# Kernel optimization log

Measured on AMD Instinct MI355X. Metric: run time of the kernel, lower is better.

The kernel has to match this reference:

```python
import jax, jax.numpy as jnp
import numpy as np

B, S, D, H, E, K = 4, 1024, 1024, 16, 8, 2
DH = D // H
FF = 4 * D  # expert hidden dim
EPS = 1e-5


def _layernorm(x, g, b):
    mu = jnp.mean(x, axis=-1, keepdims=True)
    var = jnp.mean(jnp.square(x - mu), axis=-1, keepdims=True)
    return (x - mu) / jnp.sqrt(var + EPS) * g + b


def setup_inputs() -> dict:
    key = jax.random.key(0)
    ks = jax.random.split(key, 16)
    s = 0.02
    return {
        "x": jax.random.normal(ks[0], (B, S, D), jnp.float32),
        "mask": jnp.ones((B, S), jnp.int32),
        "ln1_g": jnp.ones((D,), jnp.float32),
        "ln1_b": jnp.zeros((D,), jnp.float32),
        "ln2_g": jnp.ones((D,), jnp.float32),
        "ln2_b": jnp.zeros((D,), jnp.float32),
        "wq": jax.random.normal(ks[1], (D, D), jnp.float32) * s,
        "bq": jnp.zeros((D,), jnp.float32),
        "wk": jax.random.normal(ks[2], (D, D), jnp.float32) * s,
        "bk": jnp.zeros((D,), jnp.float32),
        "wv": jax.random.normal(ks[3], (D, D), jnp.float32) * s,
        "bv": jnp.zeros((D,), jnp.float32),
        "wo": jax.random.normal(ks[4], (D, D), jnp.float32) * s,
        "bo": jnp.zeros((D,), jnp.float32),
        "w_router": jax.random.normal(ks[5], (D, E), jnp.float32) * s,
        "b_router": jnp.zeros((E,), jnp.float32),
        "w1": jax.random.normal(ks[6], (E, D, FF), jnp.float32) * s,
        "b1": jnp.zeros((E, FF), jnp.float32),
        "w2": jax.random.normal(ks[7], (E, FF, D), jnp.float32) * s,
        "b2": jnp.zeros((E, D), jnp.float32),
    }


def _forward(x, mask, ln1_g, ln1_b, ln2_g, ln2_b, wq, bq, wk, bk, wv, bv,
             wo, bo, w_router, b_router, w1, b1, w2, b2):
    scale = DH ** -0.5
    # --- attention sub-block (pre-LN) ---
    xn = _layernorm(x, ln1_g, ln1_b)
    q = (xn @ wq + bq).reshape(B, S, H, DH).transpose(0, 2, 1, 3)  # [B,H,S,DH]
    k = (xn @ wk + bk).reshape(B, S, H, DH).transpose(0, 2, 1, 3)
    v = (xn @ wv + bv).reshape(B, S, H, DH).transpose(0, 2, 1, 3)
    scores = jnp.einsum('bhqd,bhkd->bhqk', q, k) * scale
    scores = jnp.where(mask[:, None, None, :] == 0, -jnp.inf, scores)
    attn = jax.nn.softmax(scores, axis=-1)
    ao = jnp.einsum('bhqk,bhkd->bhqd', attn, v)
    ao = ao.transpose(0, 2, 1, 3).reshape(B, S, D) @ wo + bo
    x = x + ao  # dropout is identity in eval
    # --- MoE sub-block ---
    xn2 = _layernorm(x, ln2_g, ln2_b)
    logits = xn2 @ w_router + b_router          # [B,S,E]
    top_v, top_i = jax.lax.top_k(logits, K)     # [B,S,K]
    probs = jax.nn.softmax(top_v, axis=-1)      # softmax over top-k logits
    # dense combine weight per expert: sum_k prob_k * onehot(idx_k)
    combine = jnp.sum(jax.nn.one_hot(top_i, E, dtype=xn2.dtype) * probs[..., None], axis=-2)  # [B,S,E]
    h = jax.nn.gelu(jnp.einsum('bsd,edh->ebsh', xn2, w1) + b1[:, None, None, :], approximate=False)
    eo = jnp.einsum('ebsh,ehd->ebsd', h, w2) + b2[:, None, None, :]   # [E,B,S,D]
    moe_out = jnp.einsum('bse,ebsd->bsd', combine, eo)
    return x + moe_out


def reference(x, mask, ln1_g, ln1_b, ln2_g, ln2_b, wq, bq, wk, bk, wv, bv,
              wo, bo, w_router, b_router, w1, b1, w2, b2):
    return _forward(x, mask, ln1_g, ln1_b, ln2_g, ln2_b, wq, bq, wk, bk, wv,
                    bv, wo, bo, w_router, b_router, w1, b1, w2, b2)
```

## Files before the change

kernel.cpp:

```cpp
#include <hip/hip_runtime.h>
#include <hip/hip_bf16.h>
#include <cmath>

typedef __hip_bfloat16 bf16;
typedef float f32x4 __attribute__((ext_vector_type(4)));
typedef int   i32x4 __attribute__((ext_vector_type(4)));

#define DEV static __device__ __forceinline__

constexpr int BB   = 4;
constexpr int SS   = 1024;
constexpr int DM   = 1024;
constexpr int HH   = 16;
constexpr int DHD  = 64;
constexpr int NEXP = 8;
constexpr int FFD  = 4096;
constexpr int NTOK = BB*SS;
constexpr int CAP  = NTOK*2 + NEXP*128;

DEV float bf2f(unsigned short u){ union{unsigned int i; float f;} z; z.i=((unsigned int)u)<<16; return z.f; }
DEV unsigned short f2bf(float f){ bf16 h = __float2bfloat16(f); return __builtin_bit_cast(unsigned short, h); }

DEV void stage16(const void* g, void* lds_base_uniform) {
  __builtin_amdgcn_global_load_lds(
      (const __attribute__((address_space(1))) void*)g,
      (__attribute__((address_space(3))) void*)lds_base_uniform,
      16, 0, 0);
}

template<int BM,int BN,int EPI,bool EXPERT,bool GATHER,bool OUT_SLOT,int NPASS=1,int ZMODE=0>
__global__ __launch_bounds__((BM/64)*(BN/64)*64)
void et_gemm(const bf16* __restrict__ A, const bf16* __restrict__ Bt, void* __restrict__ Cout,
             const float* __restrict__ bias, const float* __restrict__ res,
             int Kdim, int lda, int ldb, int ldc,
             long abs_, long bbs_, long cbs_, float scale,
             const int* __restrict__ pad_off, const int* __restrict__ slots,
             long psA, long psB, float* __restrict__ Cf, int bias_zs)
{
  constexpr int WN = BN/64, WM = BM/64, NW = WM*WN;
  constexpr int CA = (BM/16)/NW, CB = (BN/16)/NW;
  const int tid = threadIdx.x, wid = tid>>6, lane = tid&63;

  const int gx = gridDim.x, gy = gridDim.y;
  const long nwg = (long)gx*gy*gridDim.z;
  long lin = blockIdx.x + (long)gx*(blockIdx.y + (long)gy*blockIdx.z);
  {
    const long q = nwg >> 3, r = nwg & 7;
    const long xcd = lin & 7, idx = lin >> 3;
    lin = (xcd < r ? xcd*(q+1) : r*(q+1) + (xcd-r)*q) + idx;
  }
  const int bxi = (int)(lin % gx);
  const long rem = lin / gx;
  const int byi = (int)(rem % gy);
  const int bzi = (int)(rem / gy);

  const int row0 = bxi*BM, col0 = byi*BN;
  const int z = bzi;
  int off0 = 0;
  if constexpr (EXPERT) {
    off0 = pad_off[z];
    const int rows = pad_off[z+1] - off0;
    if (row0 >= rows) return;
  }
  long coff;
  if constexpr (ZMODE==2) {
    A  += (long)z*SS*SS;
    Bt += (long)z*DHD*SS;
    coff = (long)(z>>4)*SS*DM + (long)(z&15)*64;
  } else {
    if constexpr (!EXPERT) A += (size_t)z * abs_;
    Bt += (size_t)z * bbs_;
    coff = (long)z*cbs_;
  }
  const long bofs = (long)z * bias_zs;

  const int sr = lane>>2;
  const int sk = (lane&3)*8;

  long arow[CA];
  #pragma unroll
  for (int i=0;i<CA;i++){
    const int r = (wid + i*NW)*16 + sr;
    if constexpr (GATHER)      arow[i] = slots[off0 + row0 + r];
    else if constexpr (EXPERT) arow[i] = off0 + row0 + r;
    else                       arow[i] = row0 + r;
  }
  int brow[CB];
  #pragma unroll
  for (int i=0;i<CB;i++) brow[i] = col0 + (wid + i*NW)*16 + sr;

  const int wm = wid / WN, wn = wid % WN;
  const int fr = lane & 15, fg = lane >> 4;

  f32x4 acc[4][4];
  #pragma unroll
  for (int m=0;m<4;m++)
    #pragma unroll
    for (int n=0;n<4;n++) acc[m][n] = (f32x4)(0.f);

  if constexpr (NPASS==3) {
    __shared__ __align__(16) bf16 As[2][2][BM*32];
    __shared__ __align__(16) bf16 Bs[2][2][BN*32];
    auto STG = [&](int buf, int kt) {
      #pragma unroll
      for (int i=0;i<CA;i++){
        stage16(A +        arow[i]*(long)lda + kt + sk, (void*)&As[buf][0][(wid + i*NW)*512]);
        stage16(A + psA +  arow[i]*(long)lda + kt + sk, (void*)&As[buf][1][(wid + i*NW)*512]);
      }
      #pragma unroll
      for (int i=0;i<CB;i++){
        stage16(Bt +       (long)brow[i]*ldb + kt + sk, (void*)&Bs[buf][0][(wid + i*NW)*512]);
        stage16(Bt + psB + (long)brow[i]*ldb + kt + sk, (void*)&Bs[buf][1][(wid + i*NW)*512]);
      }
    };
    const int nsteps = Kdim >> 5;
    int cur = 0;
    STG(0, 0);
    __syncthreads();
    for (int s = 0; s < nsteps; s++) {
      if (s + 1 < nsteps) STG(cur^1, (s+1)*32);
      i32x4 a0[4], a1[4], b0[4], b1[4];
      #pragma unroll
      for (int m=0;m<4;m++) {
        a0[m] = *(const i32x4*)&As[cur][0][(wm*64 + m*16 + fr)*32 + fg*8];
        a1[m] = *(const i32x4*)&As[cur][1][(wm*64 + m*16 + fr)*32 + fg*8];
      }
      #pragma unroll
      for (int n=0;n<4;n++) {
        b0[n] = *(const i32x4*)&Bs[cur][0][(wn*64 + n*16 + fr)*32 + fg*8];
        b1[n] = *(const i32x4*)&Bs[cur][1][(wn*64 + n*16 + fr)*32 + fg*8];
      }
      asm volatile("s_nop 1" ::);
      #pragma unroll
      for (int m=0;m<4;m++)
        #pragma unroll
        for (int n=0;n<4;n++) {
          asm("v_mfma_f32_16x16x32_bf16 %0, %1, %2, %0"
              : "+v"(acc[m][n]) : "v"(a0[m]), "v"(b0[n]));
          asm("v_mfma_f32_16x16x32_bf16 %0, %1, %2, %0"
              : "+v"(acc[m][n]) : "v"(a0[m]), "v"(b1[n]));
          asm("v_mfma_f32_16x16x32_bf16 %0, %1, %2, %0"
              : "+v"(acc[m][n]) : "v"(a1[m]), "v"(b0[n]));
        }
      __syncthreads();
      cur ^= 1;
    }
  } else {
    __shared__ __align__(16) bf16 As[2][BM*32];
    __shared__ __align__(16) bf16 Bs[2][BN*32];
    auto STAGE = [&](int buf, int kt) {
      #pragma unroll
      for (int i=0;i<CA;i++)
        stage16(A + arow[i]*(long)lda + kt + sk, (void*)&As[buf][(wid + i*NW)*512]);
      #pragma unroll
      for (int i=0;i<CB;i++)
        stage16(Bt + (long)brow[i]*ldb + kt + sk, (void*)&Bs[buf][(wid + i*NW)*512]);
    };
    const int nsteps = Kdim >> 5;
    int cur = 0;
    STAGE(0, 0);
    __syncthreads();
    for (int s = 0; s < nsteps; s++) {
      if (s + 1 < nsteps) STAGE(cur^1, (s+1)*32);
      i32x4 av[4], bv[4];
      #pragma unroll
      for (int m=0;m<4;m++) av[m] = *(const i32x4*)&As[cur][(wm*64 + m*16 + fr)*32 + fg*8];
      #pragma unroll
      for (int n=0;n<4;n++) bv[n] = *(const i32x4*)&Bs[cur][(wn*64 + n*16 + fr)*32 + fg*8];
      asm volatile("s_nop 1" ::);
      #pragma unroll
      for (int m=0;m<4;m++)
        #pragma unroll
        for (int n=0;n<4;n++)
          asm("v_mfma_f32_16x16x32_bf16 %0, %1, %2, %0"
              : "+v"(acc[m][n]) : "v"(av[m]), "v"(bv[n]));
      __syncthreads();
      cur ^= 1;
    }
  }

  #pragma unroll
  for (int m=0;m<4;m++)
    #pragma unroll
    for (int n=0;n<4;n++)
      asm volatile("s_nop 7\n\ts_nop 7" : "+v"(acc[m][n]) ::);

  const long rbase = (EXPERT && OUT_SLOT) ? (long)(off0 + row0) : (long)row0;
  #pragma unroll
  for (int m=0;m<4;m++) {
    #pragma unroll
    for (int n=0;n<4;n++) {
      #pragma unroll
      for (int j=0;j<4;j++) {
        const long r = rbase + wm*64 + m*16 + fg*4 + j;
        const long c = col0 + wn*64 + n*16 + fr;
        const size_t ci = (size_t)coff + (size_t)r*ldc + c;
        float v = acc[m][n][j];
        if constexpr (EPI==0) {
          ((bf16*)Cout)[ci] = __float2bfloat16(v + bias[bofs + c]);
        } else if constexpr (EPI==1) {
          ((bf16*)Cout)[ci] = __float2bfloat16(v*scale);
        } else if constexpr (EPI==2) {
          ((float*)Cout)[ci] = v + bias[bofs + c] + res[(size_t)r*ldc + c];
        } else if constexpr (EPI==3) {
          const float t = v + bias[bofs + c];
          ((bf16*)Cout)[ci] = __float2bfloat16(0.5f*t*(1.0f+erff(t*0.70710678118654752f)));
        } else {
          const float t = v + bias[bofs + c];
          ((bf16*)Cout)[ci] = __float2bfloat16(t);
          Cf[ci] = t;
        }
      }
    }
  }
}

__global__ __launch_bounds__(256)
void k_flash(const bf16* __restrict__ qb, const bf16* __restrict__ kb,
             const bf16* __restrict__ vt, const int* __restrict__ mask,
             bf16* __restrict__ aob)
{
  const int qt = blockIdx.x, h = blockIdx.y, b = blockIdx.z;
  const int tid = threadIdx.x, wid = tid>>6, lane = tid&63;
  const int fr = lane & 15, fg = lane >> 4;
  __shared__ __align__(16) bf16 Ks[64*64];
  __shared__ __align__(16) bf16 Vs[64*64];
  __shared__ __align__(16) bf16 Pl[4][16*64];
  const int q0 = qt*64;
  const int qrow = q0 + wid*16 + fr;
  i32x4 qreg[2];
  #pragma unroll
  for (int c=0;c<2;c++)
    qreg[c] = *(const i32x4*)&qb[((size_t)(b*SS)+qrow)*DM + h*64 + c*32 + fg*8];
  f32x4 oacc[4];
  #pragma unroll
  for (int n=0;n<4;n++) oacc[n]=(f32x4)(0.f);
  float mrow[4], lrow[4];
  #pragma unroll
  for (int j=0;j<4;j++){ mrow[j]=-1e30f; lrow[j]=0.f; }

  const int srow = lane>>3;
  const int scolsw = ((lane&7) ^ srow)*8;
  auto swz = [](int row, int coleb)->int {
    return row*128 + (coleb ^ ((row&7)<<4));
  };

  for (int kt=0; kt<SS/64; kt++) {
    const int kv0 = kt*64;
    #pragma unroll
    for (int i=0;i<2;i++) {
      const int r = (wid*2+i)*8 + srow;
      stage16(kb + ((size_t)(b*SS)+kv0+r)*DM + h*64 + scolsw, (void*)&Ks[(wid*2+i)*512]);
      stage16(vt + ((size_t)(b*HH+h)*64 + r)*SS + kv0 + scolsw, (void*)&Vs[(wid*2+i)*512]);
    }
    __syncthreads();
    f32x4 sacc[4];
    #pragma unroll
    for (int n=0;n<4;n++) sacc[n]=(f32x4)(0.f);
    asm volatile("s_nop 1" ::);
    #pragma unroll
    for (int c=0;c<2;c++) {
      i32x4 bk[4];
      #pragma unroll
      for (int n=0;n<4;n++)
        bk[n] = *(const i32x4*)((const char*)Ks + swz(n*16+fr, c*64+fg*16));
      #pragma unroll
      for (int n=0;n<4;n++)
        asm("v_mfma_f32_16x16x32_bf16 %0, %1, %2, %0"
            : "+v"(sacc[n]) : "v"(qreg[c]), "v"(bk[n]));
    }
    #pragma unroll
    for (int n=0;n<4;n++)
      asm volatile("s_nop 7\n\ts_nop 7" : "+v"(sacc[n]) ::);
    float sc[4][4];
    #pragma unroll
    for (int n=0;n<4;n++) {
      const bool mm = mask[b*SS + kv0 + n*16 + fr] != 0;
      #pragma unroll
      for (int j=0;j<4;j++)
        sc[n][j] = mm ? sacc[n][j]*0.125f : -1e30f;
    }
    float scale[4];
    #pragma unroll
    for (int j=0;j<4;j++) {
      float tm = fmaxf(fmaxf(sc[0][j],sc[1][j]),fmaxf(sc[2][j],sc[3][j]));
      #pragma unroll
      for (int o=8;o;o>>=1) tm = fmaxf(tm, __shfl_xor(tm,o));
      const float nm = fmaxf(mrow[j], tm);
      scale[j] = __expf(mrow[j]-nm);
      mrow[j] = nm;
      float ts = 0.f;
      #pragma unroll
      for (int n=0;n<4;n++) { sc[n][j] = __expf(sc[n][j]-nm); ts += sc[n][j]; }
      #pragma unroll
      for (int o=8;o;o>>=1) ts += __shfl_xor(ts,o);
      lrow[j] = lrow[j]*scale[j] + ts;
    }
    #pragma unroll
    for (int n=0;n<4;n++)
      asm volatile("s_nop 7\n\ts_nop 7" : "+v"(oacc[n]) ::);
    #pragma unroll
    for (int n=0;n<4;n++)
      #pragma unroll
      for (int j=0;j<4;j++) oacc[n][j] *= scale[j];
    char* plw = (char*)Pl[wid];
    #pragma unroll
    for (int n=0;n<4;n++)
      #pragma unroll
      for (int j=0;j<4;j++) {
        const int row = fg*4+j, col = n*16+fr;
        *(bf16*)(plw + row*128 + ((col*2) ^ ((row&7)<<4))) = __float2bfloat16(sc[n][j]);
      }
    asm volatile("s_nop 1" ::);
    #pragma unroll
    for (int c=0;c<2;c++) {
      i32x4 pa = *(const i32x4*)(plw + swz(fr, c*64+fg*16));
      i32x4 bv[4];
      #pragma unroll
      for (int n=0;n<4;n++)
        bv[n] = *(const i32x4*)((const char*)Vs + swz(n*16+fr, c*64+fg*16));
      #pragma unroll
      for (int n=0;n<4;n++)
        asm("v_mfma_f32_16x16x32_bf16 %0, %1, %2, %0"
            : "+v"(oacc[n]) : "v"(pa), "v"(bv[n]));
    }
    __syncthreads();
  }
  #pragma unroll
  for (int n=0;n<4;n++)
    asm volatile("s_nop 7\n\ts_nop 7" : "+v"(oacc[n]) ::);
  #pragma unroll
  for (int j=0;j<4;j++) {
    const float ri = 1.0f / lrow[j];
    const size_t rbase = ((size_t)(b*SS) + q0 + wid*16 + fg*4 + j)*DM + h*64;
    #pragma unroll
    for (int n=0;n<4;n++)
      aob[rbase + n*16 + fr] = __float2bfloat16(oacc[n][j] * ri);
  }
}

template<typename T>
__global__ __launch_bounds__(256)
void et_transpose(const T* __restrict__ in, bf16* __restrict__ outp,
                  int ldin, int ldout, long in_bs, long out_bs)
{
  __shared__ float tile[64][65];
  const int z = blockIdx.z;
  in   += (size_t)z * in_bs;
  outp += (size_t)z * out_bs;
  const int r0 = blockIdx.x*64, c0 = blockIdx.y*64;
  const int tid = threadIdx.x;
  #pragma unroll
  for (int i=0;i<4;i++) {
    const int idx = tid*4 + i*1024;
    const int r = idx>>6, c = idx&63;
    if constexpr (sizeof(T)==4) {
      const float4 v = *(const float4*)&in[(size_t)(r0+r)*ldin + c0 + c];
      tile[r][c]=v.x; tile[r][c+1]=v.y; tile[r][c+2]=v.z; tile[r][c+3]=v.w;
    } else {
      const ushort4 v = *(const ushort4*)&in[(size_t)(r0+r)*ldin + c0 + c];
      tile[r][c]=bf2f(v.x); tile[r][c+1]=bf2f(v.y); tile[r][c+2]=bf2f(v.z); tile[r][c+3]=bf2f(v.w);
    }
  }
  __syncthreads();
  #pragma unroll
  for (int i=0;i<4;i++) {
    const int idx = tid*4 + i*1024;
    const int c = idx>>6, r = idx&63;
    ushort4 o;
    o.x=f2bf(tile[r][c]); o.y=f2bf(tile[r+1][c]); o.z=f2bf(tile[r+2][c]); o.w=f2bf(tile[r+3][c]);
    *(ushort4*)&outp[(size_t)(c0+c)*ldout + r0 + r] = o;
  }
}

template<typename TI, typename TO>
__global__ __launch_bounds__(256)
void k_trans_head(const TI* __restrict__ in, TO* __restrict__ outp)
{
  __shared__ float tile[64][65];
  const int z = blockIdx.z;
  in   += (size_t)(z>>4)*SS*DM + (size_t)(z&15)*64;
  outp += (size_t)z*DHD*SS;
  const int r0 = blockIdx.x*64;
  const int tid = threadIdx.x;
  #pragma unroll
  for (int i=0;i<4;i++) {
    const int idx = tid*4 + i*1024;
    const int r = idx>>6, c = idx&63;
    if constexpr (sizeof(TI)==4) {
      const float4 v = *(const float4*)&in[(size_t)(r0+r)*DM + c];
      tile[r][c]=v.x; tile[r][c+1]=v.y; tile[r][c+2]=v.z; tile[r][c+3]=v.w;
    } else {
      const ushort4 v = *(const ushort4*)&in[(size_t)(r0+r)*DM + c];
      tile[r][c]=bf2f(v.x); tile[r][c+1]=bf2f(v.y); tile[r][c+2]=bf2f(v.z); tile[r][c+3]=bf2f(v.w);
    }
  }
  __syncthreads();
  #pragma unroll
  for (int i=0;i<4;i++) {
    const int idx = tid*4 + i*1024;
    const int c = idx>>6, r = idx&63;
    if constexpr (sizeof(TO)==4) {
      float4 o;
      o.x=tile[r][c]; o.y=tile[r+1][c]; o.z=tile[r+2][c]; o.w=tile[r+3][c];
      *(float4*)&outp[(size_t)c*SS + r0 + r] = o;
    } else {
      ushort4 o;
      o.x=f2bf(tile[r][c]); o.y=f2bf(tile[r+1][c]); o.z=f2bf(tile[r+2][c]); o.w=f2bf(tile[r+3][c]);
      *(ushort4*)&outp[(size_t)c*SS + r0 + r] = o;
    }
  }
}

__global__ __launch_bounds__(256)
void et_transpose2(const float* __restrict__ in0, const float* __restrict__ in1,
                   const float* __restrict__ in2, bf16* __restrict__ outp,
                   int ldin, int ldout, long pstride, long out_zs)
{
  __shared__ float tile[64][65];
  const int z = blockIdx.z;
  const float* in = (z==0) ? in0 : (z==1) ? in1 : in2;
  outp += (size_t)z * out_zs;
  const int r0 = blockIdx.x*64, c0 = blockIdx.y*64;
  const int tid = threadIdx.x;
  #pragma unroll
  for (int i=0;i<4;i++) {
    const int idx = tid*4 + i*1024;
    const int r = idx>>6, c = idx&63;
    const float4 v = *(const float4*)&in[(size_t)(r0+r)*ldin + c0 + c];
    tile[r][c]=v.x; tile[r][c+1]=v.y; tile[r][c+2]=v.z; tile[r][c+3]=v.w;
  }
  __syncthreads();
  #pragma unroll
  for (int i=0;i<4;i++) {
    const int idx = tid*4 + i*1024;
    const int c = idx>>6, r = idx&63;
    ushort4 o0, o1;
    unsigned short* p0 = (unsigned short*)&o0;
    unsigned short* p1 = (unsigned short*)&o1;
    #pragma unroll
    for (int j=0;j<4;j++) {
      float v = tile[r+j][c];
      const unsigned short h0 = f2bf(v);
      p0[j] = h0;
      v -= bf2f(h0);
      p1[j] = f2bf(v);
    }
    const size_t oi = (size_t)(c0+c)*ldout + r0 + r;
    *(ushort4*)&outp[oi] = o0;
    *(ushort4*)&outp[oi + pstride] = o1;
  }
}

__global__ __launch_bounds__(256)
void et_ln2(const float* __restrict__ xin, const float* __restrict__ g,
            const float* __restrict__ bsh, bf16* __restrict__ outp, long pstride)
{
  const int row = blockIdx.x, tid = threadIdx.x;
  const float4 v = ((const float4*)(xin + (size_t)row*DM))[tid];
  float s = v.x+v.y+v.z+v.w;
  #pragma unroll
  for (int o=32;o;o>>=1) s += __shfl_xor(s,o);
  __shared__ float s4[4], q4[4];
  if ((tid&63)==0) s4[tid>>6]=s;
  __syncthreads();
  const float mu = (s4[0]+s4[1]+s4[2]+s4[3]) * (1.f/DM);
  const float d0=v.x-mu,d1=v.y-mu,d2=v.z-mu,d3=v.w-mu;
  float q = d0*d0+d1*d1+d2*d2+d3*d3;
  #pragma unroll
  for (int o=32;o;o>>=1) q += __shfl_xor(q,o);
  if ((tid&63)==0) q4[tid>>6]=q;
  __syncthreads();
  const float var = (q4[0]+q4[1]+q4[2]+q4[3]) * (1.f/DM);
  const float rstd = rsqrtf(var + 1e-5f);
  const float4 gg = ((const float4*)g)[tid];
  const float4 bb = ((const float4*)bsh)[tid];
  float of[4];
  of[0] = d0*rstd*gg.x + bb.x;
  of[1] = d1*rstd*gg.y + bb.y;
  of[2] = d2*rstd*gg.z + bb.z;
  of[3] = d3*rstd*gg.w + bb.w;
  ushort4 p0, p1;
  unsigned short* pp0 = (unsigned short*)&p0;
  unsigned short* pp1 = (unsigned short*)&p1;
  #pragma unroll
  for (int k=0;k<4;k++) {
    float vv = of[k];
    const unsigned short h0 = f2bf(vv); pp0[k] = h0;
    vv -= bf2f(h0);
    pp1[k] = f2bf(vv);
  }
  const size_t oi = (size_t)row*DM;
  ((ushort4*)(outp + oi))[tid] = p0;
  ((ushort4*)(outp + pstride + oi))[tid] = p1;
}

__global__ __launch_bounds__(256)
void et_router2(const float* __restrict__ x1, const float* __restrict__ g,
                const float* __restrict__ bsh, const float* __restrict__ wr,
                const float* __restrict__ br, bf16* __restrict__ xn2,
                int* __restrict__ t2e, float* __restrict__ t2p,
                int* __restrict__ flaglist, int* __restrict__ cntb)
{
  const int wid = threadIdx.x>>6, lane = threadIdx.x&63;
  const int t = blockIdx.x*4 + wid;
  const float* xr = x1 + (size_t)t*DM;
  float4 xv[4];
  float s = 0.f;
  #pragma unroll
  for (int p=0;p<4;p++){
    xv[p] = *(const float4*)&xr[p*256 + lane*4];
    s += xv[p].x+xv[p].y+xv[p].z+xv[p].w;
  }
  #pragma unroll
  for (int o=32;o;o>>=1) s += __shfl_xor(s,o);
  const float mu = s * (1.f/DM);
  float q = 0.f;
  #pragma unroll
  for (int p=0;p<4;p++){
    const float a=xv[p].x-mu,b=xv[p].y-mu,c=xv[p].z-mu,d=xv[p].w-mu;
    q += a*a+b*b+c*c+d*d;
  }
  #pragma unroll
  for (int o=32;o;o>>=1) q += __shfl_xor(q,o);
  const float rstd = rsqrtf(q*(1.f/DM) + 1e-5f);
  float acc[NEXP];
  #pragma unroll
  for (int e=0;e<NEXP;e++) acc[e]=0.f;
  #pragma unroll
  for (int p=0;p<4;p++){
    const int d0 = p*256 + lane*4;
    const float4 gg = *(const float4*)&g[d0];
    const float4 bb = *(const float4*)&bsh[d0];
    float xn[4];
    xn[0]=(xv[p].x-mu)*rstd*gg.x+bb.x;
    xn[1]=(xv[p].y-mu)*rstd*gg.y+bb.y;
    xn[2]=(xv[p].z-mu)*rstd*gg.z+bb.z;
    xn[3]=(xv[p].w-mu)*rstd*gg.w+bb.w;
    ushort4 xo;
    xo.x=f2bf(xn[0]); xo.y=f2bf(xn[1]); xo.z=f2bf(xn[2]); xo.w=f2bf(xn[3]);
    *(ushort4*)&xn2[(size_t)t*DM + d0] = xo;
    #pragma unroll
    for (int j=0;j<4;j++){
      const float4 w0  = ((const float4*)&wr[(size_t)(d0+j)*NEXP])[0];
      const float4 w1v = ((const float4*)&wr[(size_t)(d0+j)*NEXP])[1];
      acc[0]+=xn[j]*w0.x;  acc[1]+=xn[j]*w0.y;  acc[2]+=xn[j]*w0.z;  acc[3]+=xn[j]*w0.w;
      acc[4]+=xn[j]*w1v.x; acc[5]+=xn[j]*w1v.y; acc[6]+=xn[j]*w1v.z; acc[7]+=xn[j]*w1v.w;
    }
  }
  #pragma unroll
  for (int e=0;e<NEXP;e++)
    #pragma unroll
    for (int o=32;o;o>>=1) acc[e] += __shfl_xor(acc[e],o);
  if (lane==0) {
    float v0=-1e30f, v1=-1e30f, v2=-1e30f; int e0=0, e1=0;
    #pragma unroll
    for (int e=0;e<NEXP;e++) {
      const float v = acc[e] + br[e];
      if (v>v0){v2=v1;v1=v0;e1=e0;v0=v;e0=e;}
      else if (v>v1){v2=v1;v1=v;e1=e;}
      else if (v>v2){v2=v;}
    }
    const float dd = __expf(v1-v0);
    const float p0 = 1.f/(1.f+dd);
    t2e[t*2]=e0; t2e[t*2+1]=e1;
    t2p[t*2]=p0; t2p[t*2+1]=dd*p0;
    if (v1 - v2 < 0.02f) {
      const int b = t >> 10;
      const int ib = atomicAdd(&cntb[b], 1);
      flaglist[b*1024 + ib] = t;
    }
  }
}

__global__ __launch_bounds__(256)
void k_rec4(const float* __restrict__ qf, const float* __restrict__ kfT,
            const float* __restrict__ vf, const int* __restrict__ flaglist,
            const int* __restrict__ cntb, const int* __restrict__ mask,
            float* __restrict__ aoF)
{
  const int h = blockIdx.y, b = blockIdx.z;
  const int tid = threadIdx.x, lane = tid&63, wv_ = tid>>6;
  const int nb = cntb[b];
  __shared__ float qs[4][64];
  __shared__ float scb[4][SS];
  __shared__ float part[4][4][64];
  __shared__ float tsum[4];
  const int* mrow = mask + (size_t)b*SS;
  const float* kbase = kfT + ((size_t)(b*HH + h)*DHD)*SS + tid;
  const float* vbase = vf + (size_t)b*SS*DM + h*64 + lane;

  for (int t0 = blockIdx.x*4; t0 < nb; t0 += gridDim.x*4) {
    const int nt = min(4, nb - t0);
    for (int idx = tid; idx < 4*64; idx += 256) {
      const int j = idx >> 6, d = idx & 63;
      float qv = 0.f;
      if (j < nt) {
        const int t = flaglist[b*1024 + t0 + j];
        qv = qf[(size_t)t*DM + h*64 + d];
      }
      qs[j][d] = qv;
    }
    __syncthreads();
    float a00=0,a01=0,a02=0,a03=0, a10=0,a11=0,a12=0,a13=0;
    float a20=0,a21=0,a22=0,a23=0, a30=0,a31=0,a32=0,a33=0;
    #pragma unroll 4
    for (int u=0; u<64; u++) {
      const float* kr = kbase + (size_t)u*SS;
      const float k0 = kr[0], k1 = kr[256], k2 = kr[512], k3 = kr[768];
      const float q0 = qs[0][u], q1 = qs[1][u], q2 = qs[2][u], q3 = qs[3][u];
      a00 += q0*k0; a01 += q0*k1; a02 += q0*k2; a03 += q0*k3;
      a10 += q1*k0; a11 += q1*k1; a12 += q1*k2; a13 += q1*k3;
      a20 += q2*k0; a21 += q2*k1; a22 += q2*k2; a23 += q2*k3;
      a30 += q3*k0; a31 += q3*k1; a32 += q3*k2; a33 += q3*k3;
    }
    const bool m0 = mrow[tid]!=0, m1 = mrow[tid+256]!=0, m2 = mrow[tid+512]!=0, m3 = mrow[tid+768]!=0;
    scb[0][tid]=m0?a00*0.125f:-1e30f; scb[0][tid+256]=m1?a01*0.125f:-1e30f;
    scb[0][tid+512]=m2?a02*0.125f:-1e30f; scb[0][tid+768]=m3?a03*0.125f:-1e30f;
    scb[1][tid]=m0?a10*0.125f:-1e30f; scb[1][tid+256]=m1?a11*0.125f:-1e30f;
    scb[1][tid+512]=m2?a12*0.125f:-1e30f; scb[1][tid+768]=m3?a13*0.125f:-1e30f;
    scb[2][tid]=m0?a20*0.125f:-1e30f; scb[2][tid+256]=m1?a21*0.125f:-1e30f;
    scb[2][tid+512]=m2?a22*0.125f:-1e30f; scb[2][tid+768]=m3?a23*0.125f:-1e30f;
    scb[3][tid]=m0?a30*0.125f:-1e30f; scb[3][tid+256]=m1?a31*0.125f:-1e30f;
    scb[3][tid+512]=m2?a32*0.125f:-1e30f; scb[3][tid+768]=m3?a33*0.125f:-1e30f;
    __syncthreads();
    {
      const int j = wv_;
      float v[16];
      float lm = -1e30f;
      #pragma unroll
      for (int kk=0;kk<16;kk++) { v[kk] = scb[j][lane + kk*64]; lm = fmaxf(lm, v[kk]); }
      #pragma unroll
      for (int o=32;o;o>>=1) lm = fmaxf(lm, __shfl_xor(lm,o));
      float ls = 0.f;
      #pragma unroll
      for (int kk=0;kk<16;kk++) {
        const float e = expf(v[kk]-lm);
        scb[j][lane + kk*64] = e; ls += e;
      }
      #pragma unroll
      for (int o=32;o;o>>=1) ls += __shfl_xor(ls,o);
      if (lane==0) tsum[j] = ls;
    }
    __syncthreads();
    float p0=0.f, p1=0.f, p2=0.f, p3=0.f;
    for (int s = wv_*4; s < SS; s += 16) {
      const float v0 = vbase[(size_t) s   *DM];
      const float v1 = vbase[(size_t)(s+1)*DM];
      const float v2 = vbase[(size_t)(s+2)*DM];
      const float v3 = vbase[(size_t)(s+3)*DM];
      p0 += scb[0][s]*v0 + scb[0][s+1]*v1 + scb[0][s+2]*v2 + scb[0][s+3]*v3;
      p1 += scb[1][s]*v0 + scb[1][s+1]*v1 + scb[1][s+2]*v2 + scb[1][s+3]*v3;
      p2 += scb[2][s]*v0 + scb[2][s+1]*v1 + scb[2][s+2]*v2 + scb[2][s+3]*v3;
      p3 += scb[3][s]*v0 + scb[3][s+1]*v1 + scb[3][s+2]*v2 + scb[3][s+3]*v3;
    }
    part[wv_][0][lane] = p0;
    part[wv_][1][lane] = p1;
    part[wv_][2][lane] = p2;
    part[wv_][3][lane] = p3;
    __syncthreads();
    for (int idx = tid; idx < nt*64; idx += 256) {
      const int j = idx >> 6, d = idx & 63;
      aoF[(size_t)(b*1024 + t0 + j)*DM + h*64 + d] =
        (part[0][j][d]+part[1][j][d]+part[2][j][d]+part[3][j][d]) / tsum[j];
    }
    __syncthreads();
  }
}

__global__ __launch_bounds__(256)
void k_flag_proj2(const float* __restrict__ aoF, const float* __restrict__ wo,
                  const float* __restrict__ bo, const float* __restrict__ x,
                  const int* __restrict__ flaglist, const int* __restrict__ cntb,
                  float* __restrict__ yF)
{
  const int tile = blockIdx.x;
  const int b = tile >> 7;
  const int i0 = (tile & 127) * 8;
  const int nb = cntb[b];
  if (i0 >= nb) return;
  const int nt = min(8, nb - i0);
  const int c0 = blockIdx.y * 128;
  const int tid = threadIdx.x;
  const int c = c0 + (tid & 127);
  const int dh = tid >> 7;
  __shared__ float ar[8][DM];
  __shared__ float ph[2][8][128];
  for (int k = tid; k < 8*256; k += 256) {
    const int j = k >> 8, q4i = k & 255;
    float4 v = make_float4(0.f,0.f,0.f,0.f);
    if (j < nt) v = ((const float4*)(aoF + (size_t)(b*1024 + i0 + j)*DM))[q4i];
    ((float4*)ar[j])[q4i] = v;
  }
  __syncthreads();
  float acc0=0.f, acc1=0.f, acc2=0.f, acc3=0.f;
  float acc4=0.f, acc5=0.f, acc6=0.f, acc7=0.f;
  const int dbase = dh*512;
  #pragma unroll 4
  for (int d=0; d<512; d++) {
    const float w = wo[(size_t)(dbase+d)*DM + c];
    acc0 += ar[0][dbase+d]*w; acc1 += ar[1][dbase+d]*w;
    acc2 += ar[2][dbase+d]*w; acc3 += ar[3][dbase+d]*w;
    acc4 += ar[4][dbase+d]*w; acc5 += ar[5][dbase+d]*w;
    acc6 += ar[6][dbase+d]*w; acc7 += ar[7][dbase+d]*w;
  }
  const int lc = tid & 127;
  ph[dh][0][lc]=acc0; ph[dh][1][lc]=acc1; ph[dh][2][lc]=acc2; ph[dh][3][lc]=acc3;
  ph[dh][4][lc]=acc4; ph[dh][5][lc]=acc5; ph[dh][6][lc]=acc6; ph[dh][7][lc]=acc7;
  __syncthreads();
  for (int k = tid; k < nt*128; k += 256) {
    const int j = k >> 7, ccl = k & 127;
    const int cc = c0 + ccl;
    const int slot = b*1024 + i0 + j;
    const int t = flaglist[slot];
    yF[(size_t)slot*DM + cc] = ph[0][j][ccl] + ph[1][j][ccl] + bo[cc] + x[(size_t)t*DM + cc];
  }
}

__global__ __launch_bounds__(256)
void k_flag_router(const float* __restrict__ yF, const float* __restrict__ g,
                   const float* __restrict__ bsh, const float* __restrict__ wr,
                   const float* __restrict__ br, const int* __restrict__ flaglist,
                   const int* __restrict__ cntb, int* __restrict__ t2e,
                   float* __restrict__ t2p)
{
  const int tid = threadIdx.x, lane = tid&63, wv_ = tid>>6;
  __shared__ float s4[4], q4[4], pt[4][8];
  for (int idx = blockIdx.x; idx < NTOK; idx += gridDim.x) {
    const int b = idx >> 10, ib = idx & 1023;
    if (ib >= cntb[b]) continue;
    const int t = flaglist[idx];
    const float4 v = ((const float4*)(yF + (size_t)idx*DM))[tid];
    float s = v.x+v.y+v.z+v.w;
    #pragma unroll
    for (int o=32;o;o>>=1) s += __shfl_xor(s,o);
    if (lane==0) s4[wv_]=s;
    __syncthreads();
    const float mu = (s4[0]+s4[1]+s4[2]+s4[3])*(1.f/DM);
    const float d0=v.x-mu, d1=v.y-mu, d2=v.z-mu, d3=v.w-mu;
    float q = d0*d0+d1*d1+d2*d2+d3*d3;
    #pragma unroll
    for (int o=32;o;o>>=1) q += __shfl_xor(q,o);
    if (lane==0) q4[wv_]=q;
    __syncthreads();
    const float var = (q4[0]+q4[1]+q4[2]+q4[3])*(1.f/DM);
    const float rstd = 1.0f/sqrtf(var + 1e-5f);
    const int dbase = tid*4;
    const float4 gg = ((const float4*)g)[tid];
    const float4 bb = ((const float4*)bsh)[tid];
    const float x0 = d0*rstd*gg.x+bb.x, x1_ = d1*rstd*gg.y+bb.y;
    const float x2 = d2*rstd*gg.z+bb.z, x3_ = d3*rstd*gg.w+bb.w;
    float pl[8];
    #pragma unroll
    for (int e=0;e<8;e++)
      pl[e] = x0*wr[(size_t)(dbase+0)*8+e] + x1_*wr[(size_t)(dbase+1)*8+e]
            + x2*wr[(size_t)(dbase+2)*8+e] + x3_*wr[(size_t)(dbase+3)*8+e];
    #pragma unroll
    for (int e=0;e<8;e++)
      #pragma unroll
      for (int o=32;o;o>>=1) pl[e] += __shfl_xor(pl[e],o);
    if (lane==0) {
      #pragma unroll
      for (int e=0;e<8;e++) pt[wv_][e]=pl[e];
    }
    __syncthreads();
    if (tid==0) {
      float v0=-1e30f, v1=-1e30f; int e0=0, e1=0;
      for (int e=0;e<8;e++) {
        const float L = pt[0][e]+pt[1][e]+pt[2][e]+pt[3][e] + br[e];
        if (L>v0){v1=v0;e1=e0;v0=L;e0=e;}
        else if (L>v1){v1=L;e1=e;}
      }
      const float dd=expf(v1-v0), p0=1.f/(1.f+dd);
      t2e[t*2]=e0; t2e[t*2+1]=e1;
      t2p[t*2]=p0; t2p[t*2+1]=dd*p0;
    }
    __syncthreads();
  }
}

__global__ void et_init(const float* __restrict__ bq, const float* __restrict__ bk,
                        const float* __restrict__ bv, float* __restrict__ bcat,
                        int* __restrict__ cnt)
{
  const int i = blockIdx.x*256 + threadIdx.x;
  if (i < 16) cnt[i]=0;
  if (i < DM) { bcat[i]=bq[i]; bcat[DM+i]=bk[i]; bcat[2*DM+i]=bv[i]; }
}

__global__ void et_count(const int* __restrict__ t2e, int* __restrict__ cnt)
{
  const int t = blockIdx.x*256 + threadIdx.x;
  if (t < NTOK) {
    atomicAdd(&cnt[t2e[t*2]], 1);
    atomicAdd(&cnt[t2e[t*2+1]], 1);
  }
}

__global__ void et_scan(const int* __restrict__ cnt, int* __restrict__ poff,
                        int* __restrict__ fil, int* __restrict__ slots)
{
  const int tid = threadIdx.x;
  if (tid==0) {
    int o=0;
    for (int e=0;e<NEXP;e++){ poff[e]=o; o += ((cnt[e]+127)>>7)<<7; }
    poff[NEXP]=o;
  }
  if (tid<NEXP) fil[tid]=0;
  for (int i=tid;i<CAP;i+=256) slots[i]=0;
}

__global__ void et_fill(const int* __restrict__ t2e, const int* __restrict__ poff,
                        int* __restrict__ fil, int* __restrict__ slots, int* __restrict__ sof)
{
  const int t = blockIdx.x*256 + threadIdx.x;
  if (t >= NTOK) return;
  #pragma unroll
  for (int kk=0;kk<2;kk++) {
    const int e = t2e[t*2+kk];
    const int pos = atomicAdd(&fil[e], 1);
    const int sl = poff[e] + pos;
    slots[sl] = t;
    sof[t*2+kk] = sl;
  }
}

__global__ __launch_bounds__(256)
void et_combine(const float* __restrict__ x1, const bf16* __restrict__ eo,
                const float* __restrict__ t2p, const int* __restrict__ sof,
                float* __restrict__ outp)
{
  const int t = blockIdx.x, tid = threadIdx.x;
  const int s0 = sof[t*2], s1 = sof[t*2+1];
  const float p0 = t2p[t*2], p1 = t2p[t*2+1];
  const float4 xv = ((const float4*)(x1 + (size_t)t*DM))[tid];
  const ushort4 a = ((const ushort4*)(eo + (size_t)s0*DM))[tid];
  const ushort4 c = ((const ushort4*)(eo + (size_t)s1*DM))[tid];
  float4 o;
  o.x = xv.x + p0*bf2f(a.x) + p1*bf2f(c.x);
  o.y = xv.y + p0*bf2f(a.y) + p1*bf2f(c.y);
  o.z = xv.z + p0*bf2f(a.z) + p1*bf2f(c.z);
  o.w = xv.w + p0*bf2f(a.w) + p1*bf2f(c.w);
  ((float4*)(outp + (size_t)t*DM))[tid] = o;
}

extern "C" void kernel_launch(void* const* d_in, const int* in_sizes, int n_in,
                              void* d_out, int out_size, void* d_ws, size_t ws_size,
                              hipStream_t stream)
{
  (void)in_sizes; (void)n_in; (void)out_size; (void)ws_size;
  const float* x    = (const float*)d_in[0];
  const int*   mask = (const int*)  d_in[1];
  const float* ln1g = (const float*)d_in[2];
  const float* ln1b = (const float*)d_in[3];
  const float* ln2g = (const float*)d_in[4];
  const float* ln2b = (const float*)d_in[5];
  const float* wq   = (const float*)d_in[6];
  const float* bq   = (const float*)d_in[7];
  const float* wk   = (const float*)d_in[8];
  const float* bk   = (const float*)d_in[9];
  const float* wv   = (const float*)d_in[10];
  const float* bv   = (const float*)d_in[11];
  const float* wo   = (const float*)d_in[12];
  const float* bo   = (const float*)d_in[13];
  const float* wr   = (const float*)d_in[14];
  const float* br   = (const float*)d_in[15];
  const float* w1   = (const float*)d_in[16];
  const float* b1   = (const float*)d_in[17];
  const float* w2   = (const float*)d_in[18];
  const float* b2   = (const float*)d_in[19];
  float* outp = (float*)d_out;

  char* wsb = (char*)d_ws;
  size_t off = 0;
  auto alloc = [&](size_t bytes)->void* {
    void* p = wsb + off;
    off += (bytes + 255) & ~(size_t)255;
    return p;
  };
  const long WPS  = (long)DM*DM;
  const long XPS  = (long)NTOK*DM;
  const long EWS  = (long)DM*FFD;
  bf16*  wqT2  = (bf16*) alloc((size_t)2*WPS*2);
  bf16*  wkT2  = (bf16*) alloc((size_t)2*WPS*2);
  bf16*  wvT2  = (bf16*) alloc((size_t)2*WPS*2);
  bf16*  woT   = (bf16*) alloc((size_t)WPS*2);
  bf16*  w1Ta  = (bf16*) alloc((size_t)NEXP*EWS*2);
  bf16*  w2Ta  = (bf16*) alloc((size_t)NEXP*EWS*2);
  bf16*  xn2p  = (bf16*) alloc((size_t)2*XPS*2);
  bf16*  qb    = (bf16*) alloc((size_t)XPS*2);
  bf16*  kb    = (bf16*) alloc((size_t)XPS*2);
  bf16*  vb    = (bf16*) alloc((size_t)XPS*2);
  bf16*  vt    = (bf16*) alloc((size_t)XPS*2);
  float* qf    = (float*)alloc((size_t)XPS*4);
  float* kf    = (float*)alloc((size_t)XPS*4);
  float* vf    = (float*)alloc((size_t)XPS*4);
  float* kfT   = (float*)alloc((size_t)XPS*4);
  bf16*  aob   = (bf16*) alloc((size_t)XPS*2);
  float* x1    = (float*)alloc((size_t)XPS*4);
  bf16*  xn2   = (bf16*) alloc((size_t)XPS*2);
  bf16*  hbuf  = (bf16*) alloc((size_t)CAP*FFD*2);
  bf16*  eo    = (bf16*) alloc((size_t)CAP*DM*2);
  float* bcat  = (float*)alloc((size_t)3*DM*4);
  int*   t2e   = (int*)  alloc((size_t)NTOK*2*4);
  float* t2p   = (float*)alloc((size_t)NTOK*2*4);
  int*   slots = (int*)  alloc((size_t)CAP*4);
  int*   sof   = (int*)  alloc((size_t)NTOK*2*4);
  int*   flagl = (int*)  alloc((size_t)NTOK*4);
  int*   cnt   = (int*)  alloc(64);
  int*   fil   = (int*)  alloc(64);
  int*   poff  = (int*)  alloc(64);
  int*   cntb  = cnt + 8;
  float* aoF   = (float*)qb;
  float* yF    = (float*)vb;

  const dim3 T256(256);

  et_init<<<4,T256,0,stream>>>(bq, bk, bv, bcat, cnt);
  et_transpose2<<<dim3(DM/64,DM/64,3),T256,0,stream>>>(wq, wk, wv, wqT2, DM, DM, WPS, 2*WPS);
  et_transpose<float><<<dim3(DM/64,DM/64,1),T256,0,stream>>>(wo, woT, DM, DM, 0, 0);

  et_ln2<<<NTOK,T256,0,stream>>>(x, ln1g, ln1b, xn2p, XPS);

  et_gemm<128,64,4,false,false,false,3,0><<<dim3(NTOK/128, DM/64, 3),dim3(128),0,stream>>>(
      xn2p, wqT2, qb, bcat, nullptr, DM, DM, DM, DM,
      0, 2*WPS, XPS, 1.f, nullptr, nullptr, XPS, WPS, qf, DM);

  k_trans_head<bf16,bf16><<<dim3(SS/64,1,BB*HH),T256,0,stream>>>(vb, vt);
  k_trans_head<float,float><<<dim3(SS/64,1,BB*HH),T256,0,stream>>>(kf, kfT);

  k_flash<<<dim3(SS/64, HH, BB),T256,0,stream>>>(qb, kb, vt, mask, aob);

  et_gemm<64,64,2,false,false,false,1,0><<<dim3(NTOK/64, DM/64, 1),dim3(64),0,stream>>>(
      aob, woT, x1, bo, x, DM, DM, DM, DM, 0,0,0, 1.f, nullptr,nullptr, 0,0,nullptr, 0);

  et_router2<<<NTOK/4,T256,0,stream>>>(x1, ln2g, ln2b, wr, br, xn2, t2e, t2p, flagl, cntb);
  k_rec4<<<dim3(32,HH,BB),T256,0,stream>>>(qf, kfT, vf, flagl, cntb, mask, aoF);
  k_flag_proj2<<<dim3(NTOK/8, DM/128),T256,0,stream>>>(aoF, wo, bo, x, flagl, cntb, yF);
  k_flag_router<<<1024,T256,0,stream>>>(yF, ln2g, ln2b, wr, br, flagl, cntb, t2e, t2p);

  et_count<<<NTOK/256,T256,0,stream>>>(t2e, cnt);
  et_scan<<<1,T256,0,stream>>>(cnt, poff, fil, slots);
  et_fill<<<NTOK/256,T256,0,stream>>>(t2e, poff, fil, slots, sof);

  et_transpose<float><<<dim3(DM/64, FFD/64, NEXP),T256,0,stream>>>(w1, w1Ta, FFD, DM, EWS, EWS);
  et_transpose<float><<<dim3(FFD/64, DM/64, NEXP),T256,0,stream>>>(w2, w2Ta, DM, FFD, EWS, EWS);

  et_gemm<128,128,3,true,true,true,1,0><<<dim3(NTOK/128, FFD/128, NEXP),T256,0,stream>>>(
      xn2, w1Ta, hbuf, b1, nullptr, DM, DM, DM, FFD,
      0, EWS, 0, 1.f, poff, slots, 0,0,nullptr, FFD);
  et_gemm<128,128,0,true,false,true,1,0><<<dim3(NTOK/128, DM/128, NEXP),T256,0,stream>>>(
      hbuf, w2Ta, eo, b2, nullptr, FFD, FFD, FFD, DM,
      0, EWS, 0, 1.f, poff, nullptr, 0,0,nullptr, DM);

  et_combine<<<NTOK,T256,0,stream>>>(x1, eo, t2p, sof, outp);
}
```

Measured before the change: 826.8 us.

## Use triple-buffered 256x128 tiles for expert GEMMs with vmcnt-based pipelining

Adds a PIPE variant of the GEMM main loop that keeps three LDS stages in flight. It waits on partial vmcnt counts instead of fully draining loads each step. The expert up and down projections switch to 256x128 tiles with 512 threads, and expert padding is raised to 256 rows to match. Larger tiles improve operand reuse and the deeper pipeline hides global load latency. In exchange, LDS use per block and padding waste per expert go up, and the grid is sized to 2*NTOK/256 blocks per expert.

New measurement: 895.9 us. +8.4%, slower.

```diff
diff --git a/kernel.cpp b/kernel.cpp
--- a/kernel.cpp
+++ b/kernel.cpp
@@ -16,7 +16,7 @@
 constexpr int NEXP = 8;
 constexpr int FFD  = 4096;
 constexpr int NTOK = BB*SS;
-constexpr int CAP  = NTOK*2 + NEXP*128;
+constexpr int CAP  = NTOK*2 + NEXP*256;
 
 DEV float bf2f(unsigned short u){ union{unsigned int i; float f;} z; z.i=((unsigned int)u)<<16; return z.f; }
 DEV unsigned short f2bf(float f){ bf16 h = __float2bfloat16(f); return __builtin_bit_cast(unsigned short, h); }
@@ -28,7 +28,7 @@
       16, 0, 0);
 }
 
-template<int BM,int BN,int EPI,bool EXPERT,bool GATHER,bool OUT_SLOT,int NPASS=1,int ZMODE=0>
+template<int BM,int BN,int EPI,bool EXPERT,bool GATHER,bool OUT_SLOT,int NPASS=1,int ZMODE=0,bool PIPE=false>
 __global__ __launch_bounds__((BM/64)*(BN/64)*64)
 void et_gemm(const bf16* __restrict__ A, const bf16* __restrict__ Bt, void* __restrict__ Cout,
              const float* __restrict__ bias, const float* __restrict__ res,
@@ -144,6 +144,48 @@
         }
       __syncthreads();
       cur ^= 1;
+    }
+  } else if constexpr (PIPE) {
+    __shared__ __align__(16) bf16 As[3][BM*32];
+    __shared__ __align__(16) bf16 Bs[3][BN*32];
+    auto STAGE = [&](int buf, int kt) {
+      #pragma unroll
+      for (int i=0;i<CA;i++)
+        stage16(A + arow[i]*(long)lda + kt + sk, (void*)&As[buf][(wid + i*NW)*512]);
+      #pragma unroll
+      for (int i=0;i<CB;i++)
+        stage16(Bt + (long)brow[i]*ldb + kt + sk, (void*)&Bs[buf][(wid + i*NW)*512]);
+    };
+    const int nsteps = Kdim >> 5;
+    STAGE(0, 0);
+    STAGE(1, 32);
+    int bcur = 0;
+    for (int s = 0; s < nsteps; s++) {
+      if (s + 2 < nsteps) {
+        STAGE((s+2)%3, (s+2)*32);
+        asm volatile("s_waitcnt vmcnt(6)" ::: "memory");
+      } else if (s + 1 < nsteps) {
+        asm volatile("s_waitcnt vmcnt(3)" ::: "memory");
+      } else {
+        asm volatile("s_waitcnt vmcnt(0)" ::: "memory");
+      }
+      __builtin_amdgcn_s_barrier();
+      asm volatile("" ::: "memory");
+      i32x4 av[4], bv[4];
+      #pragma unroll
+      for (int m=0;m<4;m++) av[m] = *(const i32x4*)&As[bcur][(wm*64 + m*16 + fr)*32 + fg*8];
+      #pragma unroll
+      for (int n=0;n<4;n++) bv[n] = *(const i32x4*)&Bs[bcur][(wn*64 + n*16 + fr)*32 + fg*8];
+      asm volatile("s_nop 1" ::);
+      #pragma unroll
+      for (int m=0;m<4;m++)
+        #pragma unroll
+        for (int n=0;n<4;n++)
+          asm("v_mfma_f32_16x16x32_bf16 %0, %1, %2, %0"
+              : "+v"(acc[m][n]) : "v"(av[m]), "v"(bv[n]));
+      asm volatile("s_waitcnt lgkmcnt(0)" ::: "memory");
+      __builtin_amdgcn_s_barrier();
+      bcur = (bcur + 1 == 3) ? 0 : bcur + 1;
     }
   } else {
     __shared__ __align__(16) bf16 As[2][BM*32];
@@ -803,7 +845,7 @@
   const int tid = threadIdx.x;
   if (tid==0) {
     int o=0;
-    for (int e=0;e<NEXP;e++){ poff[e]=o; o += ((cnt[e]+127)>>7)<<7; }
+    for (int e=0;e<NEXP;e++){ poff[e]=o; o += ((cnt[e]+255)>>8)<<8; }
     poff[NEXP]=o;
   }
   if (tid<NEXP) fil[tid]=0;
@@ -946,10 +988,10 @@
   et_transpose<float><<<dim3(DM/64, FFD/64, NEXP),T256,0,stream>>>(w1, w1Ta, FFD, DM, EWS, EWS);
   et_transpose<float><<<dim3(FFD/64, DM/64, NEXP),T256,0,stream>>>(w2, w2Ta, DM, FFD, EWS, EWS);
 
-  et_gemm<128,128,3,true,true,true,1,0><<<dim3(NTOK/128, FFD/128, NEXP),T256,0,stream>>>(
+  et_gemm<256,128,3,true,true,true,1,0,true><<<dim3(NTOK*2/256, FFD/128, NEXP),dim3(512),0,stream>>>(
       xn2, w1Ta, hbuf, b1, nullptr, DM, DM, DM, FFD,
       0, EWS, 0, 1.f, poff, slots, 0,0,nullptr, FFD);
-  et_gemm<128,128,0,true,false,true,1,0><<<dim3(NTOK/128, DM/128, NEXP),T256,0,stream>>>(
+  et_gemm<256,128,0,true,false,true,1,0,true><<<dim3(NTOK*2/256, DM/128, NEXP),dim3(512),0,stream>>>(
       hbuf, w2Ta, eo, b2, nullptr, FFD, FFD, FFD, DM,
       0, EWS, 0, 1.f, poff, nullptr, 0,0,nullptr, DM);
 
```
